# Kernel optimization log

Hardware: AMD Instinct MI355X
Metric: run time of the kernel (lower is better)

Reference implementation:

```python
import jax, jax.numpy as jnp
import numpy as np

VOCAB, EMB, H, D3, CTX = 30522, 768, 1024, 128, 512

def setup_inputs() -> dict:
    key = jax.random.key(0)
    ks = jax.random.split(key, 12)
    B, S = 8, 64
    inp = {
        'decoder_input_ids': jax.random.randint(ks[0], (B, S), 0, VOCAB, dtype=jnp.int64) if jax.config.jax_enable_x64 else jax.random.randint(ks[0], (B, S), 0, VOCAB, dtype=jnp.int32),
        'decoder_attn_mask': jnp.ones((B, S), dtype=jnp.int32),
        'decoder_seq_type_id': jnp.zeros((B, S), dtype=jnp.int32),
        'h_first': jax.random.normal(ks[1], (B, H), dtype=jnp.float32),
        'context': jax.random.normal(ks[2], (B, CTX, H), dtype=jnp.float32),
        # learned parameters (torch Linear stored transposed as [in, out])
        'emb_table': jax.random.normal(ks[3], (VOCAB, EMB), dtype=jnp.float32) * 0.02,
        'W_in': jax.random.normal(ks[4], (EMB, H), dtype=jnp.float32) * 0.02,
        'b_in': jnp.zeros((H,), dtype=jnp.float32),
        'W_s': jax.random.normal(ks[5], (H, H), dtype=jnp.float32) * 0.02,
        'b_s': jnp.zeros((H,), dtype=jnp.float32),
        'W_att_in': jax.random.normal(ks[6], (2 * H, D3), dtype=jnp.float32) * 0.02,
        'b_att_in': jnp.zeros((D3,), dtype=jnp.float32),
        'W_att_h': jax.random.normal(ks[7], (H, D3), dtype=jnp.float32) * 0.02,
        'b_att_h': jnp.zeros((D3,), dtype=jnp.float32),
        'V': jax.random.uniform(ks[8], (D3,), dtype=jnp.float32, minval=-1.0, maxval=1.0),
    }
    return inp


def reference(decoder_input_ids, decoder_attn_mask, decoder_seq_type_id, h_first,
              context, emb_table, W_in, b_in, W_s, b_s,
              W_att_in, b_att_in, W_att_h, b_att_h, V):
    # bert_embedding stub: plain token embedding lookup -> [B, S, 768]
    feats = emb_table[decoder_input_ids]
    # hidden_dense(context) is constant across steps; hoist it (same math)
    ctx_proj = context @ W_att_h + b_att_h          # [B, ctx, d3]
    h0 = context[:, -1, :]                          # initial recurrent state
    xs = jnp.swapaxes(feats, 0, 1)                  # [S, B, 768]

    def step(h, t_i):
        h = h @ W_s + b_s                           # dense_s
        s = jnp.concatenate([t_i @ W_in + b_in, h], axis=1)   # [B, 2H]
        a = jnp.tanh((s @ W_att_in + b_att_in)[:, None, :] + ctx_proj)  # [B,ctx,d3]
        att_before = jnp.einsum('d,bcd->bc', V, a)  # bmm(v, a^T) squeezed -> [B, ctx]
        # faithful to original: softmax over dim=1 of [B,1,ctx] (size-1 axis -> all ones)
        att_after = jax.nn.softmax(att_before[:, None, :], axis=1)[:, 0, :]
        idx = jnp.argmax(att_after, axis=1)         # ties -> 0, matches torch .max(1)
        return h, (att_before, idx)

    _, (atts, prts) = jax.lax.scan(step, h0, xs)
    atts = jnp.swapaxes(atts, 0, 1)                 # stack(dim=1).squeeze() -> [B, S, ctx]
    return atts, prts
```

## Files before the change

### kernel.cpp

```cpp
#include <hip/hip_runtime.h>
#include <hip/hip_bf16.h>

#define EMB 768
#define HD 1024
#define D3 128
#define CTXN 512
#define BB 8
#define SS 64

typedef __attribute__((ext_vector_type(8))) short short8v;
typedef __attribute__((ext_vector_type(4))) float f32x4;

__device__ __forceinline__ float fast_tanh(float x) {
  float e = __expf(2.f * x);
  return 1.f - 2.f * __builtin_amdgcn_rcpf(e + 1.f);
}
__device__ __forceinline__ float bf2f(__hip_bfloat16 x) { return __bfloat162float(x); }

struct GDesc {
  const void* A;
  const __hip_bfloat16* BT;
  const int* arowmap;
  const float* addrow_f;
  const float* bias_f;
  float* Cf;
  __hip_bfloat16* Cb;
  __hip_bfloat16* CbT;
  float* brow_f;
  int M, N, K, lda, ldbt, ldct, af32, mtiles, blk0, nblks;
};
struct GBatch { GDesc d[10]; int nd; };

__global__ __launch_bounds__(256) void gemmz(GBatch bat) {
  int bx = blockIdx.x;
  GDesc d = bat.d[0];
  for (int i = 1; i < bat.nd; ++i)
    if (bx >= bat.d[i].blk0) d = bat.d[i];
  int local = bx - d.blk0;
  int mt = local % d.mtiles, nt = local / d.mtiles;
  int bm0 = mt * 32, bn0 = nt * 64;

  __shared__ __hip_bfloat16 As[2][32][64];
  __shared__ __hip_bfloat16 Bs[2][64][64];
  int tid = threadIdx.x, lane = tid & 63, wid = tid >> 6;
  int l16 = lane & 15, g = lane >> 4;
  int wm = (wid & 1) * 16, wn = (wid >> 1) * 32;
  int arow = tid >> 3, aseg = tid & 7;
  int brow = tid >> 2, bseg = tid & 3;
  f32x4 acc[2] = {};

  int agr = bm0 + arow;
  int asrc = (agr < d.M) ? (d.arowmap ? d.arowmap[agr] : agr) : -1;
  const float* Af = (const float*)d.A;
  const __hip_bfloat16* Ab = (const __hip_bfloat16*)d.A;

  float fa[8];
  short8v ba = {}, bb0 = {}, bb1 = {};
  int nk = d.K >> 6;

  auto LD = [&](int k0) {
    if (d.af32) {
      if (asrc >= 0) {
        const float* s = Af + (long)asrc * d.lda + k0 + aseg * 8;
#pragma unroll
        for (int j = 0; j < 8; ++j) fa[j] = s[j];
      } else {
#pragma unroll
        for (int j = 0; j < 8; ++j) fa[j] = 0.f;
      }
    } else {
      if (asrc >= 0)
        ba = *(const short8v*)(Ab + (long)asrc * d.lda + k0 + aseg * 8);
      else {
        short8v z = {};
        ba = z;
      }
    }
    const __hip_bfloat16* bsrc = d.BT + (long)(bn0 + brow) * d.ldbt + k0 + bseg * 16;
    bb0 = *(const short8v*)bsrc;
    bb1 = *(const short8v*)(bsrc + 8);
  };
  auto ST = [&](int buf) {
    __hip_bfloat16 t8[8];
    if (d.af32) {
#pragma unroll
      for (int j = 0; j < 8; ++j) t8[j] = __float2bfloat16(fa[j]);
      *(short8v*)&As[buf][arow][(aseg ^ (arow & 7)) * 8] = *(short8v*)t8;
    } else {
      *(short8v*)&As[buf][arow][(aseg ^ (arow & 7)) * 8] = ba;
    }
    *(short8v*)&Bs[buf][brow][((2 * bseg) ^ (brow & 7)) * 8] = bb0;
    *(short8v*)&Bs[buf][brow][((2 * bseg + 1) ^ (brow & 7)) * 8] = bb1;
  };

  LD(0);
  ST(0);
  __syncthreads();
  for (int it = 0; it < nk; ++it) {
    int cur = it & 1;
    if (it + 1 < nk) LD((it + 1) << 6);
#pragma unroll
    for (int kf = 0; kf < 2; ++kf) {
      int ar = wm + l16;
      short8v a = *(const short8v*)&As[cur][ar][(((kf << 2) | g) ^ (ar & 7)) * 8];
#pragma unroll
      for (int j = 0; j < 2; ++j) {
        int br = wn + j * 16 + l16;
        short8v b = *(const short8v*)&Bs[cur][br][(((kf << 2) | g) ^ (br & 7)) * 8];
        acc[j] = __builtin_amdgcn_mfma_f32_16x16x32_bf16(a, b, acc[j], 0, 0, 0);
      }
    }
    if (it + 1 < nk) ST(cur ^ 1);
    __syncthreads();
  }

  float* Cs = (float*)&Bs[0][0][0];
  bool doT = (d.CbT != nullptr);
#pragma unroll
  for (int j = 0; j < 2; ++j)
#pragma unroll
    for (int r = 0; r < 4; ++r) {
      int gl = wm + g * 4 + r, cl = wn + j * 16 + l16;
      int grow = bm0 + gl, gcol = bn0 + cl;
      float v = acc[j][r];
      if (d.bias_f) v += d.bias_f[gcol];
      if (d.addrow_f && grow == d.M - 1) v += d.addrow_f[gcol];
      if (grow < d.M) {
        if (d.Cf) d.Cf[(long)grow * d.N + gcol] = v;
        if (d.Cb) d.Cb[(long)grow * d.N + gcol] = __float2bfloat16(v);
        if (d.brow_f && grow == d.M - 1) d.brow_f[gcol] = v;
      }
      if (doT) Cs[cl * 33 + gl] = v;
    }
  if (doT) {
    __syncthreads();
    int ctrows = d.M < 1024 ? d.M : 1024;
    int n = tid >> 2, ms = (tid & 3) * 8;
    int gm0 = bm0 + ms;
    __hip_bfloat16 t8[8];
#pragma unroll
    for (int jj = 0; jj < 8; ++jj) t8[jj] = __float2bfloat16(Cs[n * 33 + ms + jj]);
    if (gm0 + 7 < ctrows) {
      *(short8v*)&d.CbT[(long)(bn0 + n) * d.ldct + gm0] = *(short8v*)t8;
    } else {
#pragma unroll
      for (int jj = 0; jj < 8; ++jj)
        if (gm0 + jj < ctrows) d.CbT[(long)(bn0 + n) * d.ldct + gm0 + jj] = t8[jj];
    }
  }
}

__global__ __launch_bounds__(256) void kcast(const float* __restrict__ W_s,
                                             const float* __restrict__ b_s,
                                             const float* __restrict__ context,
                                             const float* __restrict__ b_in,
                                             const float* __restrict__ W_att_in,
                                             const float* __restrict__ b_att_in,
                                             const float* __restrict__ W_att_h,
                                             const int* __restrict__ ids,
                                             __hip_bfloat16* __restrict__ Mb0,
                                             __hip_bfloat16* __restrict__ Mb0T,
                                             __hip_bfloat16* __restrict__ Y0T,
                                             __hip_bfloat16* __restrict__ WahT,
                                             __hip_bfloat16* __restrict__ WaiT,
                                             __hip_bfloat16* __restrict__ Gb,
                                             float* __restrict__ qb,
                                             int* __restrict__ rowmap) {
  int blk = blockIdx.x, tid = threadIdx.x;
  __shared__ __hip_bfloat16 tl[64][65];
  __shared__ float red[2][128];

  auto TP = [&](const float* src, int R, int C, __hip_bfloat16* dst, int tr, int tc) {
    int r0 = tr * 64, c0 = tc * 64;
    {
      int r = tid >> 2, cs = (tid & 3) * 16;
      const float* s = src + (long)(r0 + r) * C + c0 + cs;
#pragma unroll
      for (int j = 0; j < 16; ++j) tl[cs + j][r] = __float2bfloat16(s[j]);
    }
    __syncthreads();
    {
      int c = tid >> 2, rs = (tid & 3) * 16;
      __hip_bfloat16 o[16];
#pragma unroll
      for (int j = 0; j < 16; ++j) o[j] = tl[c][rs + j];
      *(short8v*)&dst[(long)(c0 + c) * R + r0 + rs] = *(short8v*)&o[0];
      *(short8v*)&dst[(long)(c0 + c) * R + r0 + rs + 8] = *(short8v*)&o[8];
    }
  };

  if (blk < 256) {
    long base = (long)blk * 4096;
    for (int i = tid; i < 4096; i += 256)
      Mb0[base + i] = __float2bfloat16(W_s[base + i]);
  } else if (blk == 256) {
    for (int i = tid; i < HD; i += 256)
      Mb0[(long)HD * HD + i] = __float2bfloat16(b_s[i]);
  } else if (blk < 513) {
    int t = blk - 257;
    TP(W_s, 1024, 1024, Mb0T, t >> 4, t & 15);
  } else if (blk < 545) {
    int t = blk - 513;
    TP(W_att_in + (long)1024 * D3, 1024, 128, Y0T, t >> 1, t & 1);
  } else if (blk < 577) {
    int t = blk - 545;
    TP(W_att_h, 1024, 128, WahT, t >> 1, t & 1);
  } else if (blk < 609) {
    int t = blk - 577;
    TP(W_att_in, 1024, 128, WaiT, t >> 1, t & 1);
  } else if (blk == 609) {
    for (int i = tid; i < BB * HD; i += 256) {
      int b = i >> 10, k = i & 1023;
      Gb[i] = __float2bfloat16(context[((long)b * CTXN + CTXN - 1) * HD + k]);
    }
  } else if (blk == 610) {
    int dd = tid & 127, h = tid >> 7;
    float acc = 0.f;
    for (int k = h * 512; k < h * 512 + 512; ++k)
      acc += b_in[k] * W_att_in[k * D3 + dd];
    red[h][dd] = acc;
    __syncthreads();
    if (h == 0) qb[dd] = red[0][dd] + red[1][dd] + b_att_in[dd];
  } else {
    for (int i = tid; i < 512; i += 256) {
      int t = i >> 3, b = i & 7;
      rowmap[i] = ids[b * SS + t];
    }
  }
}

__global__ __launch_bounds__(256) void katt(const float* __restrict__ qF,
                                            const float* __restrict__ qH,
                                            const float* __restrict__ ctxp,
                                            const float* __restrict__ V,
                                            float* __restrict__ out) {
  int blk = blockIdx.x;
  int b = blk >> 5, tt = (blk >> 4) & 1, ct = blk & 15;
  int t0 = tt * 32, c0 = ct * 32;
  int tid = threadIdx.x;
  __shared__ float lq[32][128];
  __shared__ float lc[32][132];
  __shared__ float lv[128];
  for (int i = tid; i < 32 * 128; i += 256) {
    int r = i >> 7, d = i & 127;
    int t = t0 + r;
    lq[r][d] = qF[((long)t * 8 + b) * 128 + d] +
               qH[(((long)(t & 7)) * 64 + (t >> 3) * 8 + b) * 128 + d];
    lc[r][d] = ctxp[((long)b * CTXN + c0 + r) * D3 + d];
  }
  if (tid < 128) lv[tid] = V[tid];
  __syncthreads();
  int cl = tid & 31, tg = tid >> 5;
  float r[4] = {0.f, 0.f, 0.f, 0.f};
  for (int d4 = 0; d4 < 32; ++d4) {
    float4 cv = *reinterpret_cast<const float4*>(&lc[cl][d4 * 4]);
    float4 vv = *reinterpret_cast<const float4*>(&lv[d4 * 4]);
#pragma unroll
    for (int u = 0; u < 4; ++u) {
      int t = tg + u * 8;
      float4 qv = *reinterpret_cast<const float4*>(&lq[t][d4 * 4]);
      r[u] = fmaf(vv.x, fast_tanh(qv.x + cv.x), r[u]);
      r[u] = fmaf(vv.y, fast_tanh(qv.y + cv.y), r[u]);
      r[u] = fmaf(vv.z, fast_tanh(qv.z + cv.z), r[u]);
      r[u] = fmaf(vv.w, fast_tanh(qv.w + cv.w), r[u]);
    }
  }
#pragma unroll
  for (int u = 0; u < 4; ++u) {
    int t = tg + u * 8;
    out[((long)b * SS + (t0 + t)) * CTXN + c0 + cl] = r[u];
  }
  if (blk == 0) {
    for (int i = tid; i < SS * BB; i += 256) out[(long)BB * SS * CTXN + i] = 0.f;
  }
}

static inline GDesc mk(const void* A, int af32, int lda, const int* arowmap,
                       const __hip_bfloat16* BT, int ldbt, int M, int N, int K,
                       const float* addrow_f, const float* bias_f, float* Cf,
                       __hip_bfloat16* Cb, __hip_bfloat16* CbT, int ldct,
                       float* brow_f, int blk0) {
  GDesc d;
  d.A = A; d.BT = BT; d.arowmap = arowmap;
  d.addrow_f = addrow_f; d.bias_f = bias_f;
  d.Cf = Cf; d.Cb = Cb; d.CbT = CbT; d.brow_f = brow_f;
  d.M = M; d.N = N; d.K = K; d.lda = lda; d.ldbt = ldbt; d.ldct = ldct;
  d.af32 = af32;
  d.mtiles = (M + 31) >> 5;
  d.blk0 = blk0;
  d.nblks = d.mtiles * (N >> 6);
  return d;
}

extern "C" void kernel_launch(void* const* d_in, const int* in_sizes, int n_in,
                              void* d_out, int out_size, void* d_ws, size_t ws_size,
                              hipStream_t stream) {
  const int* ids = (const int*)d_in[0];
  const float* context = (const float*)d_in[4];
  const float* emb = (const float*)d_in[5];
  const float* W_in = (const float*)d_in[6];
  const float* b_in = (const float*)d_in[7];
  const float* W_s = (const float*)d_in[8];
  const float* b_s = (const float*)d_in[9];
  const float* W_att_in = (const float*)d_in[10];
  const float* b_att_in = (const float*)d_in[11];
  const float* W_att_h = (const float*)d_in[12];
  const float* b_att_h = (const float*)d_in[13];
  const float* V = (const float*)d_in[14];

  float* ws = (float*)d_ws;
  float* ctxp = ws;
  float* Yf = ctxp + 524288;
  float* qF = Yf + 1180800;
  float* qH = qF + 65536;
  float* qb = qH + 65536;
  float* brow2 = qb + 128;
  float* brow4 = brow2 + 1024;
  float* brow8 = brow4 + 1024;
  float* brow16 = brow8 + 1024;
  float* brow32 = brow16 + 1024;
  int* rowmap = (int*)(brow32 + 1024);
  __hip_bfloat16* bfp = (__hip_bfloat16*)(rowmap + 512);
  __hip_bfloat16* Mb0 = bfp;
  __hip_bfloat16* Mb0T = Mb0 + 1049600;
  __hip_bfloat16* Mb1 = Mb0T + 1048576;
  __hip_bfloat16* Mb1T = Mb1 + 1049600;
  __hip_bfloat16* Mb2 = Mb1T + 1048576;
  __hip_bfloat16* Mb2T = Mb2 + 1049600;
  __hip_bfloat16* Mb3 = Mb2T + 1048576;
  __hip_bfloat16* Mb3T = Mb3 + 1049600;
  __hip_bfloat16* YT = Mb3T + 1048576;
  __hip_bfloat16* WahT = YT + 9 * 131072;
  __hip_bfloat16* WaiT = WahT + 131072;
  __hip_bfloat16* WcT = WaiT + 131072;
  __hip_bfloat16* Gb = WcT + 131072;
  float* out = (float*)d_out;

  auto Yfr = [&](int r) { return Yf + (long)r * 131200; };
  auto YTs = [&](int r) { return YT + (long)r * 131072; };

  kcast<<<dim3(612), dim3(256), 0, stream>>>(W_s, b_s, context, b_in, W_att_in,
                                             b_att_in, W_att_h, ids, Mb0, Mb0T,
                                             YTs(0), WahT, WaiT, Gb, qb, rowmap);
  {
    GBatch bt{}; int c = 0;
    bt.d[0] = mk(Mb0, 0, 1024, nullptr, Mb0T, 1024, 1025, 1024, 1024, b_s, nullptr, nullptr, Mb1, Mb1T, 1024, brow2, c); c += bt.d[0].nblks;
    bt.d[1] = mk(Mb0, 0, 1024, nullptr, YTs(0), 1024, 1025, 128, 1024, nullptr, nullptr, Yfr(1), nullptr, YTs(1), 1024, nullptr, c); c += bt.d[1].nblks;
    bt.d[2] = mk(context, 1, 1024, nullptr, WahT, 1024, 4096, 128, 1024, nullptr, b_att_h, ctxp, nullptr, nullptr, 0, nullptr, c); c += bt.d[2].nblks;
    bt.d[3] = mk(W_in, 1, 1024, nullptr, WaiT, 1024, 768, 128, 1024, nullptr, nullptr, nullptr, nullptr, WcT, 768, nullptr, c); c += bt.d[3].nblks;
    bt.nd = 4;
    gemmz<<<dim3(c), dim3(256), 0, stream>>>(bt);
  }
  {
    GBatch bt{}; int c = 0;
    bt.d[0] = mk(Mb1, 0, 1024, nullptr, Mb1T, 1024, 1025, 1024, 1024, brow2, nullptr, nullptr, Mb2, Mb2T, 1024, brow4, c); c += bt.d[0].nblks;
    bt.d[1] = mk(Mb1, 0, 1024, nullptr, YTs(0), 1024, 1025, 128, 1024, nullptr, nullptr, Yfr(2), nullptr, YTs(2), 1024, nullptr, c); c += bt.d[1].nblks;
    bt.d[2] = mk(Mb1, 0, 1024, nullptr, YTs(1), 1024, 1025, 128, 1024, Yfr(1) + 131072, nullptr, Yfr(3), nullptr, YTs(3), 1024, nullptr, c); c += bt.d[2].nblks;
    bt.nd = 3;
    gemmz<<<dim3(c), dim3(256), 0, stream>>>(bt);
  }
  {
    GBatch bt{}; int c = 0;
    bt.d[0] = mk(Mb2, 0, 1024, nullptr, Mb2T, 1024, 1025, 1024, 1024, brow4, nullptr, nullptr, Mb3, Mb3T, 1024, brow8, c); c += bt.d[0].nblks;
    for (int s = 0; s < 4; ++s) {
      bt.d[1 + s] = mk(Mb2, 0, 1024, nullptr, YTs(s), 1024, 1025, 128, 1024,
                       (s == 0) ? nullptr : (Yfr(s) + 131072), nullptr,
                       Yfr(4 + s), nullptr, YTs(4 + s), 1024, nullptr, c);
      c += bt.d[1 + s].nblks;
    }
    bt.nd = 5;
    gemmz<<<dim3(c), dim3(256), 0, stream>>>(bt);
  }
  {
    GBatch bt{}; int c = 0;
    bt.d[0] = mk(Mb3, 0, 1024, nullptr, Mb3T, 1024, 1025, 1024, 1024, brow8, nullptr, nullptr, Mb1, Mb1T, 1024, brow16, c); c += bt.d[0].nblks;
    bt.d[1] = mk(Mb3, 0, 1024, nullptr, YTs(0), 1024, 1025, 128, 1024, nullptr, nullptr, Yfr(8), nullptr, YTs(8), 1024, nullptr, c); c += bt.d[1].nblks;
    bt.d[2] = mk(Gb, 0, 1024, nullptr, Mb3T, 1024, 8, 1024, 1024, nullptr, brow8, nullptr, Gb + 8192, nullptr, 0, nullptr, c); c += bt.d[2].nblks;
    bt.nd = 3;
    gemmz<<<dim3(c), dim3(256), 0, stream>>>(bt);
  }
  {
    GBatch bt{}; int c = 0;
    bt.d[0] = mk(Mb1, 0, 1024, nullptr, Mb1T, 1024, 1025, 1024, 1024, brow16, nullptr, nullptr, Mb2, Mb2T, 1024, brow32, c); c += bt.d[0].nblks;
    bt.d[1] = mk(Gb, 0, 1024, nullptr, Mb1T, 1024, 16, 1024, 1024, nullptr, brow16, nullptr, Gb + 16384, nullptr, 0, nullptr, c); c += bt.d[1].nblks;
    bt.nd = 2;
    gemmz<<<dim3(c), dim3(256), 0, stream>>>(bt);
  }
  {
    GBatch bt{}; int c = 0;
    bt.d[0] = mk(Gb, 0, 1024, nullptr, Mb2T, 1024, 32, 1024, 1024, nullptr, brow32, nullptr, Gb + 32768, nullptr, 0, nullptr, c); c += bt.d[0].nblks;
    bt.nd = 1;
    gemmz<<<dim3(c), dim3(256), 0, stream>>>(bt);
  }
  {
    GBatch bt{}; int c = 0;
    for (int r = 1; r <= 8; ++r) {
      bt.d[r - 1] = mk(Gb, 0, 1024, nullptr, YTs(r), 1024, 64, 128, 1024, nullptr,
                       Yfr(r) + 131072, qH + (long)(r - 1) * 8192, nullptr, nullptr,
                       0, nullptr, c);
      c += bt.d[r - 1].nblks;
    }
    bt.d[8] = mk(emb, 1, 768, rowmap, WcT, 768, 512, 128, 768, nullptr, qb, qF,
                 nullptr, nullptr, 0, nullptr, c);
    c += bt.d[8].nblks;
    bt.nd = 9;
    gemmz<<<dim3(c), dim3(256), 0, stream>>>(bt);
  }
  katt<<<dim3(256), dim3(256), 0, stream>>>(qF, qH, ctxp, V, out);
}
```

Measured before the change: 159.2 us.

## Enlarge GEMM tiles to 128x128 and compute transposes as separate GEMMs

Moves the batched GEMM kernel from 32x64 tiles to 128x128 tiles, with each wave holding a 4x4 grid of MFMA accumulators for more data reuse per shared-memory load. It drops the in-epilogue transposed bf16 output. Transposed matrix powers are now produced by extra GEMM descriptors that multiply in the transposed order. W_in is pre-cast to bf16 in the cast kernel so the combined weight is formed as a bf16 GEMM. The larger tiles mean far fewer blocks for small-N GEMMs (N=128, M=8..64), and the added transpose GEMMs roughly double the matrix-power work per launch.

Measured after the change: 266.8 us. 67.6% more time.

```diff
diff --git a/kernel.cpp b/kernel.cpp
--- a/kernel.cpp
+++ b/kernel.cpp
@@ -15,7 +15,6 @@
   float e = __expf(2.f * x);
   return 1.f - 2.f * __builtin_amdgcn_rcpf(e + 1.f);
 }
-__device__ __forceinline__ float bf2f(__hip_bfloat16 x) { return __bfloat162float(x); }
 
 struct GDesc {
   const void* A;
@@ -25,9 +24,8 @@
   const float* bias_f;
   float* Cf;
   __hip_bfloat16* Cb;
-  __hip_bfloat16* CbT;
   float* brow_f;
-  int M, N, K, lda, ldbt, ldct, af32, mtiles, blk0, nblks;
+  int M, N, K, lda, ldbt, af32, mtiles, blk0, nblks;
 };
 struct GBatch { GDesc d[10]; int nd; };
 
@@ -38,59 +36,68 @@
     if (bx >= bat.d[i].blk0) d = bat.d[i];
   int local = bx - d.blk0;
   int mt = local % d.mtiles, nt = local / d.mtiles;
-  int bm0 = mt * 32, bn0 = nt * 64;
-
-  __shared__ __hip_bfloat16 As[2][32][64];
-  __shared__ __hip_bfloat16 Bs[2][64][64];
+  int bm0 = mt * 128, bn0 = nt * 128;
+
+  __shared__ __hip_bfloat16 As[2][128][64];
+  __shared__ __hip_bfloat16 Bs[2][128][64];
   int tid = threadIdx.x, lane = tid & 63, wid = tid >> 6;
   int l16 = lane & 15, g = lane >> 4;
-  int wm = (wid & 1) * 16, wn = (wid >> 1) * 32;
-  int arow = tid >> 3, aseg = tid & 7;
-  int brow = tid >> 2, bseg = tid & 3;
-  f32x4 acc[2] = {};
-
-  int agr = bm0 + arow;
+  int wm = (wid >> 1) * 64, wn = (wid & 1) * 64;
+  int srow = tid >> 1, sseg = tid & 1;
+  f32x4 acc[4][4] = {};
+
+  int agr = bm0 + srow;
   int asrc = (agr < d.M) ? (d.arowmap ? d.arowmap[agr] : agr) : -1;
   const float* Af = (const float*)d.A;
   const __hip_bfloat16* Ab = (const __hip_bfloat16*)d.A;
 
-  float fa[8];
-  short8v ba = {}, bb0 = {}, bb1 = {};
+  float fa[32];
+  short8v ba[4], bb[4];
   int nk = d.K >> 6;
 
   auto LD = [&](int k0) {
     if (d.af32) {
       if (asrc >= 0) {
-        const float* s = Af + (long)asrc * d.lda + k0 + aseg * 8;
-#pragma unroll
-        for (int j = 0; j < 8; ++j) fa[j] = s[j];
+        const float* s = Af + (long)asrc * d.lda + k0 + sseg * 32;
+#pragma unroll
+        for (int j = 0; j < 32; ++j) fa[j] = s[j];
       } else {
 #pragma unroll
-        for (int j = 0; j < 8; ++j) fa[j] = 0.f;
+        for (int j = 0; j < 32; ++j) fa[j] = 0.f;
       }
     } else {
-      if (asrc >= 0)
-        ba = *(const short8v*)(Ab + (long)asrc * d.lda + k0 + aseg * 8);
-      else {
+      if (asrc >= 0) {
+        const __hip_bfloat16* s = Ab + (long)asrc * d.lda + k0 + sseg * 32;
+#pragma unroll
+        for (int j = 0; j < 4; ++j) ba[j] = *(const short8v*)(s + j * 8);
+      } else {
         short8v z = {};
-        ba = z;
+#pragma unroll
+        for (int j = 0; j < 4; ++j) ba[j] = z;
       }
     }
-    const __hip_bfloat16* bsrc = d.BT + (long)(bn0 + brow) * d.ldbt + k0 + bseg * 16;
-    bb0 = *(const short8v*)bsrc;
-    bb1 = *(const short8v*)(bsrc + 8);
+    const __hip_bfloat16* bs = d.BT + (long)(bn0 + srow) * d.ldbt + k0 + sseg * 32;
+#pragma unroll
+    for (int j = 0; j < 4; ++j) bb[j] = *(const short8v*)(bs + j * 8);
   };
   auto ST = [&](int buf) {
-    __hip_bfloat16 t8[8];
+    int r7 = srow & 7, c0 = sseg * 4;
     if (d.af32) {
 #pragma unroll
-      for (int j = 0; j < 8; ++j) t8[j] = __float2bfloat16(fa[j]);
-      *(short8v*)&As[buf][arow][(aseg ^ (arow & 7)) * 8] = *(short8v*)t8;
+      for (int j = 0; j < 4; ++j) {
+        __hip_bfloat16 t8[8];
+#pragma unroll
+        for (int u = 0; u < 8; ++u) t8[u] = __float2bfloat16(fa[j * 8 + u]);
+        *(short8v*)&As[buf][srow][((c0 + j) ^ r7) * 8] = *(short8v*)t8;
+      }
     } else {
-      *(short8v*)&As[buf][arow][(aseg ^ (arow & 7)) * 8] = ba;
-    }
-    *(short8v*)&Bs[buf][brow][((2 * bseg) ^ (brow & 7)) * 8] = bb0;
-    *(short8v*)&Bs[buf][brow][((2 * bseg + 1) ^ (brow & 7)) * 8] = bb1;
+#pragma unroll
+      for (int j = 0; j < 4; ++j)
+        *(short8v*)&As[buf][srow][((c0 + j) ^ r7) * 8] = ba[j];
+    }
+#pragma unroll
+    for (int j = 0; j < 4; ++j)
+      *(short8v*)&Bs[buf][srow][((c0 + j) ^ r7) * 8] = bb[j];
   };
 
   LD(0);
@@ -99,54 +106,45 @@
   for (int it = 0; it < nk; ++it) {
     int cur = it & 1;
     if (it + 1 < nk) LD((it + 1) << 6);
+    int x7 = l16 & 7;
 #pragma unroll
     for (int kf = 0; kf < 2; ++kf) {
-      int ar = wm + l16;
-      short8v a = *(const short8v*)&As[cur][ar][(((kf << 2) | g) ^ (ar & 7)) * 8];
-#pragma unroll
-      for (int j = 0; j < 2; ++j) {
-        int br = wn + j * 16 + l16;
-        short8v b = *(const short8v*)&Bs[cur][br][(((kf << 2) | g) ^ (br & 7)) * 8];
-        acc[j] = __builtin_amdgcn_mfma_f32_16x16x32_bf16(a, b, acc[j], 0, 0, 0);
-      }
+      int ch = ((kf << 2) | g) ^ x7;
+      short8v a[4], b[4];
+#pragma unroll
+      for (int f = 0; f < 4; ++f)
+        a[f] = *(const short8v*)&As[cur][wm + f * 16 + l16][ch * 8];
+#pragma unroll
+      for (int f = 0; f < 4; ++f)
+        b[f] = *(const short8v*)&Bs[cur][wn + f * 16 + l16][ch * 8];
+#pragma unroll
+      for (int fm = 0; fm < 4; ++fm)
+#pragma unroll
+        for (int fn = 0; fn < 4; ++fn)
+          acc[fm][fn] =
+              __builtin_amdgcn_mfma_f32_16x16x32_bf16(a[fm], b[fn], acc[fm][fn], 0, 0, 0);
     }
     if (it + 1 < nk) ST(cur ^ 1);
     __syncthreads();
   }
 
-  float* Cs = (float*)&Bs[0][0][0];
-  bool doT = (d.CbT != nullptr);
-#pragma unroll
-  for (int j = 0; j < 2; ++j)
-#pragma unroll
-    for (int r = 0; r < 4; ++r) {
-      int gl = wm + g * 4 + r, cl = wn + j * 16 + l16;
-      int grow = bm0 + gl, gcol = bn0 + cl;
-      float v = acc[j][r];
-      if (d.bias_f) v += d.bias_f[gcol];
-      if (d.addrow_f && grow == d.M - 1) v += d.addrow_f[gcol];
-      if (grow < d.M) {
-        if (d.Cf) d.Cf[(long)grow * d.N + gcol] = v;
-        if (d.Cb) d.Cb[(long)grow * d.N + gcol] = __float2bfloat16(v);
-        if (d.brow_f && grow == d.M - 1) d.brow_f[gcol] = v;
+#pragma unroll
+  for (int fn = 0; fn < 4; ++fn) {
+    int gcol = bn0 + wn + fn * 16 + l16;
+    float bias = d.bias_f ? d.bias_f[gcol] : 0.f;
+#pragma unroll
+    for (int fm = 0; fm < 4; ++fm)
+#pragma unroll
+      for (int r = 0; r < 4; ++r) {
+        int grow = bm0 + wm + fm * 16 + g * 4 + r;
+        if (grow < d.M) {
+          float v = acc[fm][fn][r] + bias;
+          if (d.addrow_f && grow == d.M - 1) v += d.addrow_f[gcol];
+          if (d.Cf) d.Cf[(long)grow * d.N + gcol] = v;
+          if (d.Cb) d.Cb[(long)grow * d.N + gcol] = __float2bfloat16(v);
+          if (d.brow_f && grow == d.M - 1) d.brow_f[gcol] = v;
+        }
       }
-      if (doT) Cs[cl * 33 + gl] = v;
-    }
-  if (doT) {
-    __syncthreads();
-    int ctrows = d.M < 1024 ? d.M : 1024;
-    int n = tid >> 2, ms = (tid & 3) * 8;
-    int gm0 = bm0 + ms;
-    __hip_bfloat16 t8[8];
-#pragma unroll
-    for (int jj = 0; jj < 8; ++jj) t8[jj] = __float2bfloat16(Cs[n * 33 + ms + jj]);
-    if (gm0 + 7 < ctrows) {
-      *(short8v*)&d.CbT[(long)(bn0 + n) * d.ldct + gm0] = *(short8v*)t8;
-    } else {
-#pragma unroll
-      for (int jj = 0; jj < 8; ++jj)
-        if (gm0 + jj < ctrows) d.CbT[(long)(bn0 + n) * d.ldct + gm0 + jj] = t8[jj];
-    }
   }
 }
 
@@ -157,12 +155,14 @@
                                              const float* __restrict__ W_att_in,
                                              const float* __restrict__ b_att_in,
                                              const float* __restrict__ W_att_h,
+                                             const float* __restrict__ W_in,
                                              const int* __restrict__ ids,
                                              __hip_bfloat16* __restrict__ Mb0,
                                              __hip_bfloat16* __restrict__ Mb0T,
-                                             __hip_bfloat16* __restrict__ Y0T,
+                                             __hip_bfloat16* __restrict__ Z0T,
                                              __hip_bfloat16* __restrict__ WahT,
                                              __hip_bfloat16* __restrict__ WaiT,
+                                             __hip_bfloat16* __restrict__ Winb,
                                              __hip_bfloat16* __restrict__ Gb,
                                              float* __restrict__ qb,
                                              int* __restrict__ rowmap) {
@@ -201,7 +201,7 @@
     TP(W_s, 1024, 1024, Mb0T, t >> 4, t & 15);
   } else if (blk < 545) {
     int t = blk - 513;
-    TP(W_att_in + (long)1024 * D3, 1024, 128, Y0T, t >> 1, t & 1);
+    TP(W_att_in + (long)1024 * D3, 1024, 128, Z0T, t >> 1, t & 1);
   } else if (blk < 577) {
     int t = blk - 545;
     TP(W_att_h, 1024, 128, WahT, t >> 1, t & 1);
@@ -221,11 +221,15 @@
     red[h][dd] = acc;
     __syncthreads();
     if (h == 0) qb[dd] = red[0][dd] + red[1][dd] + b_att_in[dd];
-  } else {
+  } else if (blk == 611) {
     for (int i = tid; i < 512; i += 256) {
       int t = i >> 3, b = i & 7;
       rowmap[i] = ids[b * SS + t];
     }
+  } else {
+    long base = (long)(blk - 612) * 4096;
+    for (int i = tid; i < 4096; i += 256)
+      Winb[base + i] = __float2bfloat16(W_in[base + i]);
   }
 }
 
@@ -278,17 +282,16 @@
 static inline GDesc mk(const void* A, int af32, int lda, const int* arowmap,
                        const __hip_bfloat16* BT, int ldbt, int M, int N, int K,
                        const float* addrow_f, const float* bias_f, float* Cf,
-                       __hip_bfloat16* Cb, __hip_bfloat16* CbT, int ldct,
-                       float* brow_f, int blk0) {
+                       __hip_bfloat16* Cb, float* brow_f, int blk0) {
   GDesc d;
   d.A = A; d.BT = BT; d.arowmap = arowmap;
   d.addrow_f = addrow_f; d.bias_f = bias_f;
-  d.Cf = Cf; d.Cb = Cb; d.CbT = CbT; d.brow_f = brow_f;
-  d.M = M; d.N = N; d.K = K; d.lda = lda; d.ldbt = ldbt; d.ldct = ldct;
+  d.Cf = Cf; d.Cb = Cb; d.brow_f = brow_f;
+  d.M = M; d.N = N; d.K = K; d.lda = lda; d.ldbt = ldbt;
   d.af32 = af32;
-  d.mtiles = (M + 31) >> 5;
+  d.mtiles = (M + 127) >> 7;
   d.blk0 = blk0;
-  d.nblks = d.mtiles * (N >> 6);
+  d.nblks = d.mtiles * (N >> 7);
   return d;
 }
 
@@ -333,62 +336,78 @@
   __hip_bfloat16* WahT = YT + 9 * 131072;
   __hip_bfloat16* WaiT = WahT + 131072;
   __hip_bfloat16* WcT = WaiT + 131072;
-  __hip_bfloat16* Gb = WcT + 131072;
+  __hip_bfloat16* Winb = WcT + 98304;
+  __hip_bfloat16* Gb = Winb + 786432;
   float* out = (float*)d_out;
 
   auto Yfr = [&](int r) { return Yf + (long)r * 131200; };
   auto YTs = [&](int r) { return YT + (long)r * 131072; };
-
-  kcast<<<dim3(612), dim3(256), 0, stream>>>(W_s, b_s, context, b_in, W_att_in,
-                                             b_att_in, W_att_h, ids, Mb0, Mb0T,
-                                             YTs(0), WahT, WaiT, Gb, qb, rowmap);
-  {
-    GBatch bt{}; int c = 0;
-    bt.d[0] = mk(Mb0, 0, 1024, nullptr, Mb0T, 1024, 1025, 1024, 1024, b_s, nullptr, nullptr, Mb1, Mb1T, 1024, brow2, c); c += bt.d[0].nblks;
-    bt.d[1] = mk(Mb0, 0, 1024, nullptr, YTs(0), 1024, 1025, 128, 1024, nullptr, nullptr, Yfr(1), nullptr, YTs(1), 1024, nullptr, c); c += bt.d[1].nblks;
-    bt.d[2] = mk(context, 1, 1024, nullptr, WahT, 1024, 4096, 128, 1024, nullptr, b_att_h, ctxp, nullptr, nullptr, 0, nullptr, c); c += bt.d[2].nblks;
-    bt.d[3] = mk(W_in, 1, 1024, nullptr, WaiT, 1024, 768, 128, 1024, nullptr, nullptr, nullptr, nullptr, WcT, 768, nullptr, c); c += bt.d[3].nblks;
-    bt.nd = 4;
-    gemmz<<<dim3(c), dim3(256), 0, stream>>>(bt);
-  }
-  {
-    GBatch bt{}; int c = 0;
-    bt.d[0] = mk(Mb1, 0, 1024, nullptr, Mb1T, 1024, 1025, 1024, 1024, brow2, nullptr, nullptr, Mb2, Mb2T, 1024, brow4, c); c += bt.d[0].nblks;
-    bt.d[1] = mk(Mb1, 0, 1024, nullptr, YTs(0), 1024, 1025, 128, 1024, nullptr, nullptr, Yfr(2), nullptr, YTs(2), 1024, nullptr, c); c += bt.d[1].nblks;
-    bt.d[2] = mk(Mb1, 0, 1024, nullptr, YTs(1), 1024, 1025, 128, 1024, Yfr(1) + 131072, nullptr, Yfr(3), nullptr, YTs(3), 1024, nullptr, c); c += bt.d[2].nblks;
+  const long MB = 1024L * 1024;
+
+  kcast<<<dim3(804), dim3(256), 0, stream>>>(W_s, b_s, context, b_in, W_att_in,
+                                             b_att_in, W_att_h, W_in, ids, Mb0,
+                                             Mb0T, YTs(0), WahT, WaiT, Winb, Gb,
+                                             qb, rowmap);
+  {
+    GBatch bt{}; int c = 0;
+    bt.d[0] = mk(Mb0, 0, 1024, nullptr, Mb0T, 1024, 1025, 1024, 1024, b_s, nullptr, nullptr, Mb1, brow2, c); c += bt.d[0].nblks;
+    bt.d[1] = mk(Mb0T, 0, 1024, nullptr, Mb0, 1024, 1024, 1024, 1024, nullptr, nullptr, nullptr, Mb1T, nullptr, c); c += bt.d[1].nblks;
+    bt.d[2] = mk(Mb0, 0, 1024, nullptr, YTs(0), 1024, 1025, 128, 1024, nullptr, nullptr, Yfr(1), nullptr, nullptr, c); c += bt.d[2].nblks;
+    bt.d[3] = mk(YTs(0), 0, 1024, nullptr, Mb0, 1024, 128, 1024, 1024, nullptr, nullptr, nullptr, YTs(1), nullptr, c); c += bt.d[3].nblks;
+    bt.d[4] = mk(context, 1, 1024, nullptr, WahT, 1024, 4096, 128, 1024, nullptr, b_att_h, ctxp, nullptr, nullptr, c); c += bt.d[4].nblks;
+    bt.d[5] = mk(WaiT, 0, 1024, nullptr, Winb, 1024, 128, 768, 1024, nullptr, nullptr, nullptr, WcT, nullptr, c); c += bt.d[5].nblks;
+    bt.nd = 6;
+    gemmz<<<dim3(c), dim3(256), 0, stream>>>(bt);
+  }
+  {
+    GBatch bt{}; int c = 0;
+    bt.d[0] = mk(Mb1, 0, 1024, nullptr, Mb1T, 1024, 1025, 1024, 1024, brow2, nullptr, nullptr, Mb2, brow4, c); c += bt.d[0].nblks;
+    bt.d[1] = mk(Mb1T, 0, 1024, nullptr, Mb1, 1024, 1024, 1024, 1024, nullptr, nullptr, nullptr, Mb2T, nullptr, c); c += bt.d[1].nblks;
+    bt.d[2] = mk(Mb1, 0, 1024, nullptr, YTs(0), 1024, 1025, 128, 1024, nullptr, nullptr, Yfr(2), nullptr, nullptr, c); c += bt.d[2].nblks;
+    bt.d[3] = mk(YTs(0), 0, 1024, nullptr, Mb1, 1024, 128, 1024, 1024, nullptr, nullptr, nullptr, YTs(2), nullptr, c); c += bt.d[3].nblks;
+    bt.d[4] = mk(Mb1, 0, 1024, nullptr, YTs(1), 1024, 1025, 128, 1024, Yfr(1) + 131072, nullptr, Yfr(3), nullptr, nullptr, c); c += bt.d[4].nblks;
+    bt.d[5] = mk(YTs(1), 0, 1024, nullptr, Mb1, 1024, 128, 1024, 1024, nullptr, nullptr, nullptr, YTs(3), nullptr, c); c += bt.d[5].nblks;
+    bt.nd = 6;
+    gemmz<<<dim3(c), dim3(256), 0, stream>>>(bt);
+  }
+  {
+    GBatch bt{}; int c = 0;
+    bt.d[0] = mk(Mb2, 0, 1024, nullptr, Mb2T, 1024, 1025, 1024, 1024, brow4, nullptr, nullptr, Mb3, brow8, c); c += bt.d[0].nblks;
+    bt.d[1] = mk(Mb2T, 0, 1024, nullptr, Mb2, 1024, 1024, 1024, 1024, nullptr, nullptr, nullptr, Mb3T, nullptr, c); c += bt.d[1].nblks;
+    int k = 2;
+    for (int s = 0; s < 4; ++s) {
+      bt.d[k] = mk(Mb2, 0, 1024, nullptr, YTs(s), 1024, 1025, 128, 1024,
+                   (s == 0) ? nullptr : (Yfr(s) + 131072), nullptr, Yfr(4 + s),
+                   nullptr, nullptr, c);
+      c += bt.d[k].nblks; ++k;
+      bt.d[k] = mk(YTs(s), 0, 1024, nullptr, Mb2, 1024, 128, 1024, 1024, nullptr,
+                   nullptr, nullptr, YTs(4 + s), nullptr, c);
+      c += bt.d[k].nblks; ++k;
+    }
+    bt.nd = 10;
+    gemmz<<<dim3(c), dim3(256), 0, stream>>>(bt);
+  }
+  {
+    GBatch bt{}; int c = 0;
+    bt.d[0] = mk(Mb3, 0, 1024, nullptr, Mb3T, 1024, 1025, 1024, 1024, brow8, nullptr, nullptr, Mb1, brow16, c); c += bt.d[0].nblks;
+    bt.d[1] = mk(Mb3T, 0, 1024, nullptr, Mb3, 1024, 1024, 1024, 1024, nullptr, nullptr, nullptr, Mb1T, nullptr, c); c += bt.d[1].nblks;
+    bt.d[2] = mk(Mb3, 0, 1024, nullptr, YTs(0), 1024, 1025, 128, 1024, nullptr, nullptr, Yfr(8), nullptr, nullptr, c); c += bt.d[2].nblks;
+    bt.d[3] = mk(YTs(0), 0, 1024, nullptr, Mb3, 1024, 128, 1024, 1024, nullptr, nullptr, nullptr, YTs(8), nullptr, c); c += bt.d[3].nblks;
+    bt.d[4] = mk(Gb, 0, 1024, nullptr, Mb3T, 1024, 8, 1024, 1024, nullptr, brow8, nullptr, Gb + 8192, nullptr, c); c += bt.d[4].nblks;
+    bt.nd = 5;
+    gemmz<<<dim3(c), dim3(256), 0, stream>>>(bt);
+  }
+  {
+    GBatch bt{}; int c = 0;
+    bt.d[0] = mk(Mb1T, 0, 1024, nullptr, Mb1, 1024, 1024, 1024, 1024, nullptr, nullptr, nullptr, Mb2T, nullptr, c); c += bt.d[0].nblks;
+    bt.d[1] = mk(Mb1 + MB, 0, 1024, nullptr, Mb1T, 1024, 1, 1024, 1024, nullptr, brow16, brow32, nullptr, nullptr, c); c += bt.d[1].nblks;
+    bt.d[2] = mk(Gb, 0, 1024, nullptr, Mb1T, 1024, 16, 1024, 1024, nullptr, brow16, nullptr, Gb + 16384, nullptr, c); c += bt.d[2].nblks;
     bt.nd = 3;
     gemmz<<<dim3(c), dim3(256), 0, stream>>>(bt);
   }
   {
     GBatch bt{}; int c = 0;
-    bt.d[0] = mk(Mb2, 0, 1024, nullptr, Mb2T, 1024, 1025, 1024, 1024, brow4, nullptr, nullptr, Mb3, Mb3T, 1024, brow8, c); c += bt.d[0].nblks;
-    for (int s = 0; s < 4; ++s) {
-      bt.d[1 + s] = mk(Mb2, 0, 1024, nullptr, YTs(s), 1024, 1025, 128, 1024,
-                       (s == 0) ? nullptr : (Yfr(s) + 131072), nullptr,
-                       Yfr(4 + s), nullptr, YTs(4 + s), 1024, nullptr, c);
-      c += bt.d[1 + s].nblks;
-    }
-    bt.nd = 5;
-    gemmz<<<dim3(c), dim3(256), 0, stream>>>(bt);
-  }
-  {
-    GBatch bt{}; int c = 0;
-    bt.d[0] = mk(Mb3, 0, 1024, nullptr, Mb3T, 1024, 1025, 1024, 1024, brow8, nullptr, nullptr, Mb1, Mb1T, 1024, brow16, c); c += bt.d[0].nblks;
-    bt.d[1] = mk(Mb3, 0, 1024, nullptr, YTs(0), 1024, 1025, 128, 1024, nullptr, nullptr, Yfr(8), nullptr, YTs(8), 1024, nullptr, c); c += bt.d[1].nblks;
-    bt.d[2] = mk(Gb, 0, 1024, nullptr, Mb3T, 1024, 8, 1024, 1024, nullptr, brow8, nullptr, Gb + 8192, nullptr, 0, nullptr, c); c += bt.d[2].nblks;
-    bt.nd = 3;
-    gemmz<<<dim3(c), dim3(256), 0, stream>>>(bt);
-  }
-  {
-    GBatch bt{}; int c = 0;
-    bt.d[0] = mk(Mb1, 0, 1024, nullptr, Mb1T, 1024, 1025, 1024, 1024, brow16, nullptr, nullptr, Mb2, Mb2T, 1024, brow32, c); c += bt.d[0].nblks;
-    bt.d[1] = mk(Gb, 0, 1024, nullptr, Mb1T, 1024, 16, 1024, 1024, nullptr, brow16, nullptr, Gb + 16384, nullptr, 0, nullptr, c); c += bt.d[1].nblks;
-    bt.nd = 2;
-    gemmz<<<dim3(c), dim3(256), 0, stream>>>(bt);
-  }
-  {
-    GBatch bt{}; int c = 0;
-    bt.d[0] = mk(Gb, 0, 1024, nullptr, Mb2T, 1024, 32, 1024, 1024, nullptr, brow32, nullptr, Gb + 32768, nullptr, 0, nullptr, c); c += bt.d[0].nblks;
+    bt.d[0] = mk(Gb, 0, 1024, nullptr, Mb2T, 1024, 32, 1024, 1024, nullptr, brow32, nullptr, Gb + 32768, nullptr, c); c += bt.d[0].nblks;
     bt.nd = 1;
     gemmz<<<dim3(c), dim3(256), 0, stream>>>(bt);
   }
@@ -396,12 +415,11 @@
     GBatch bt{}; int c = 0;
     for (int r = 1; r <= 8; ++r) {
       bt.d[r - 1] = mk(Gb, 0, 1024, nullptr, YTs(r), 1024, 64, 128, 1024, nullptr,
-                       Yfr(r) + 131072, qH + (long)(r - 1) * 8192, nullptr, nullptr,
-                       0, nullptr, c);
+                       Yfr(r) + 131072, qH + (long)(r - 1) * 8192, nullptr, nullptr, c);
       c += bt.d[r - 1].nblks;
     }
     bt.d[8] = mk(emb, 1, 768, rowmap, WcT, 768, 512, 128, 768, nullptr, qb, qF,
-                 nullptr, nullptr, 0, nullptr, c);
+                 nullptr, nullptr, c);
     c += bt.d[8].nblks;
     bt.nd = 9;
     gemmz<<<dim3(c), dim3(256), 0, stream>>>(bt);
```
